# Performance work log

Hardware: AMD Instinct MI355X
Metric: run time of the kernel (lower is better)

## Reference

```python
import jax, jax.numpy as jnp
import numpy as np

GAMMA = 0.5  # RBF bandwidth, matches init_kwargs gamma


def setup_inputs() -> dict:
    key = jax.random.key(0)
    x = jax.random.normal(key, (8192, 64), dtype=jnp.float32)
    return {"x": x}


def reference(x):
    # Gram[i, j] = exp(-gamma * ||x_i - x_j||^2), computed fully batched.
    # ||xi - xj||^2 = ||xi||^2 + ||xj||^2 - 2 <xi, xj>
    sq = jnp.sum(x * x, axis=-1)                      # [n]
    d2 = sq[:, None] + sq[None, :] - 2.0 * (x @ x.T)  # [n, n]
    d2 = jnp.maximum(d2, 0.0)                         # numerical floor
    out = jnp.exp(-GAMMA * d2)                        # [n, n]
    n = x.shape[0]
    return out.reshape(n, -1)
```

## Files before the change

### kernel.cpp

```cpp
#include <hip/hip_runtime.h>


#define GAMMA 0.5f

typedef __attribute__((ext_vector_type(8))) _Float16 half8;
typedef __attribute__((ext_vector_type(4))) float f32x4;

__global__ __launch_bounds__(256) void quant_kernel(const float* __restrict__ x,
                                                    unsigned short* __restrict__ H,
                                                    float* __restrict__ sq) {
    int tid = blockIdx.x * 256 + threadIdx.x;
    int row = tid >> 4, c4 = tid & 15;
    float4 v = ((const float4*)x)[tid];
    float e[4] = {v.x, v.y, v.z, v.w};
    unsigned short hb[4];
    float s = 0.f;
    #pragma unroll
    for (int i = 0; i < 4; ++i) {
        _Float16 h = (_Float16)e[i];
        float hf = (float)h;
        s = fmaf(hf, hf, s);
        hb[i] = __builtin_bit_cast(unsigned short, h);
    }
    int rr = row & 127;
    size_t base = (size_t)(row >> 7) * 16384;
    int b = (rr * 128 + c4 * 8) ^ ((rr & 7) << 4);
    uint2 hw = {(unsigned)hb[0] | ((unsigned)hb[1] << 16),
                (unsigned)hb[2] | ((unsigned)hb[3] << 16)};
    *(uint2*)((char*)H + base + b) = hw;
    s += __shfl_xor(s, 1); s += __shfl_xor(s, 2);
    s += __shfl_xor(s, 4); s += __shfl_xor(s, 8);
    if (c4 == 0) sq[row] = s;
}

__global__ __launch_bounds__(256, 4) void rbf_mfma12(const unsigned short* __restrict__ H,
                                                     const float* __restrict__ sq,
                                                     float* __restrict__ out, int N) {
    __shared__ __align__(16) char smem[32768];
    unsigned short* Ah = (unsigned short*)smem;
    unsigned short* Bh = (unsigned short*)(smem + 16384);

    const int tid = threadIdx.x;
    const int i0 = blockIdx.y * 128, j0 = blockIdx.x * 128;
    const int w = tid >> 6, lane = tid & 63;
    const int fr = lane & 15, kg = lane >> 4;
    const int wr = w * 32;

    {
        const uint4* ga = (const uint4*)(H + (size_t)i0 * 64);
        const uint4* gb = (const uint4*)(H + (size_t)j0 * 64);
        #pragma unroll
        for (int t = 0; t < 4; ++t) {
            ((uint4*)Ah)[t * 256 + tid] = ga[t * 256 + tid];
            ((uint4*)Bh)[t * 256 + tid] = gb[t * 256 + tid];
        }
    }
    __syncthreads();

    f32x4 acc[2][8];
    #pragma unroll
    for (int p = 0; p < 2; ++p)
        #pragma unroll
        for (int q = 0; q < 8; ++q) acc[p][q] = (f32x4)(0.f);

    #pragma unroll
    for (int ks = 0; ks < 2; ++ks) {
        const int kb = ks * 64 + kg * 16;
        half8 ah[2], bh[8];
        #pragma unroll
        for (int p = 0; p < 2; ++p) {
            int R = wr + p * 16 + fr;
            int off = (R * 128 + kb) ^ ((R & 7) << 4);
            ah[p] = *(const half8*)((const char*)Ah + off);
        }
        #pragma unroll
        for (int q = 0; q < 8; ++q) {
            int R = q * 16 + fr;
            int off = (R * 128 + kb) ^ ((R & 7) << 4);
            bh[q] = *(const half8*)((const char*)Bh + off);
        }
        #pragma unroll
        for (int p = 0; p < 2; ++p)
            #pragma unroll
            for (int q = 0; q < 8; ++q)
                acc[p][q] = __builtin_amdgcn_mfma_f32_16x16x32_f16(bh[q], ah[p], acc[p][q], 0, 0, 0);
    }

    __syncthreads();
    float* wbuf = (float*)smem + w * 2048;

    #pragma unroll
    for (int p = 0; p < 2; ++p) {
        float sa = sq[i0 + wr + p * 16 + fr];
        #pragma unroll
        for (int q = 0; q < 8; ++q) {
            int c = q * 16 + kg * 4;
            float4 sb = *(const float4*)&sq[j0 + c];
            f32x4 a = acc[p][q];
            f32x4 r;
            r[0] = __expf(-GAMMA * fmaxf(fmaf(-2.f, a[0], sa + sb.x), 0.f));
            r[1] = __expf(-GAMMA * fmaxf(fmaf(-2.f, a[1], sa + sb.y), 0.f));
            r[2] = __expf(-GAMMA * fmaxf(fmaf(-2.f, a[2], sa + sb.z), 0.f));
            r[3] = __expf(-GAMMA * fmaxf(fmaf(-2.f, a[3], sa + sb.w), 0.f));
            *(f32x4*)&wbuf[fr * 128 + (c ^ ((fr & 7) << 2))] = r;
        }
        const int half = lane >> 5, lc = lane & 31;
        #pragma unroll
        for (int i = 0; i < 8; ++i) {
            int rl = i * 2 + half;
            f32x4 v = *(const f32x4*)&wbuf[rl * 128 + ((lc * 4) ^ ((rl & 7) << 2))];
            int grow = i0 + wr + p * 16 + rl;
            __builtin_nontemporal_store(v, (f32x4*)(out + (size_t)grow * N + j0 + lc * 4));
        }
    }
}

extern "C" void kernel_launch(void* const* d_in, const int* in_sizes, int n_in,
                              void* d_out, int out_size, void* d_ws, size_t ws_size,
                              hipStream_t stream) {
    (void)n_in; (void)ws_size; (void)out_size;
    const float* x = (const float*)d_in[0];
    float* out = (float*)d_out;
    const int K = 64;
    const int N = in_sizes[0] / K;

    unsigned short* H = (unsigned short*)d_ws;
    float* sq = (float*)(H + (size_t)N * K);

    quant_kernel<<<dim3(N * K / 4 / 256), dim3(256), 0, stream>>>(x, H, sq);
    rbf_mfma12<<<dim3(N / 128, N / 128), dim3(256), 0, stream>>>(H, sq, out, N);
}
```

Before: 55.91 us.

## Reshape tiles to 64x256 and write full 1KB output rows per wave

Changes the block tile from 128x128 to 64 rows by 256 columns. Each wave now computes a 16x256 strip, with a single A fragment reused across 16 MFMAs. The epilogue stages 8 rows at a time in LDS so each store instruction writes a contiguous 1KB row segment. Nontemporal stores become regular stores, and sched barriers plus an explicit lgkmcnt wait order the LDS phases. The B tile load doubles while the A tile halves, and the LDS footprint grows to 40KB, which may cut occupancy.

```diff
diff --git a/kernel.cpp b/kernel.cpp
--- a/kernel.cpp
+++ b/kernel.cpp
@@ -33,84 +33,78 @@
     if (c4 == 0) sq[row] = s;
 }
 
-__global__ __launch_bounds__(256, 4) void rbf_mfma12(const unsigned short* __restrict__ H,
+__global__ __launch_bounds__(256, 4) void rbf_mfma14(const unsigned short* __restrict__ H,
                                                      const float* __restrict__ sq,
                                                      float* __restrict__ out, int N) {
-    __shared__ __align__(16) char smem[32768];
+    __shared__ __align__(16) char smem[40960];
     unsigned short* Ah = (unsigned short*)smem;
-    unsigned short* Bh = (unsigned short*)(smem + 16384);
+    unsigned short* Bh = (unsigned short*)(smem + 8192);
 
     const int tid = threadIdx.x;
-    const int i0 = blockIdx.y * 128, j0 = blockIdx.x * 128;
+    const int i0 = blockIdx.y * 64, j0 = blockIdx.x * 256;
     const int w = tid >> 6, lane = tid & 63;
     const int fr = lane & 15, kg = lane >> 4;
-    const int wr = w * 32;
 
     {
         const uint4* ga = (const uint4*)(H + (size_t)i0 * 64);
         const uint4* gb = (const uint4*)(H + (size_t)j0 * 64);
         #pragma unroll
-        for (int t = 0; t < 4; ++t) {
+        for (int t = 0; t < 2; ++t)
             ((uint4*)Ah)[t * 256 + tid] = ga[t * 256 + tid];
+        #pragma unroll
+        for (int t = 0; t < 8; ++t)
             ((uint4*)Bh)[t * 256 + tid] = gb[t * 256 + tid];
-        }
     }
     __syncthreads();
 
-    f32x4 acc[2][8];
+    f32x4 acc[16];
     #pragma unroll
-    for (int p = 0; p < 2; ++p)
-        #pragma unroll
-        for (int q = 0; q < 8; ++q) acc[p][q] = (f32x4)(0.f);
+    for (int q = 0; q < 16; ++q) acc[q] = (f32x4)(0.f);
 
     #pragma unroll
     for (int ks = 0; ks < 2; ++ks) {
         const int kb = ks * 64 + kg * 16;
-        half8 ah[2], bh[8];
+        int Ra = w * 16 + fr;
+        half8 ah = *(const half8*)((const char*)Ah + ((Ra * 128 + kb) ^ ((Ra & 7) << 4)));
         #pragma unroll
-        for (int p = 0; p < 2; ++p) {
-            int R = wr + p * 16 + fr;
-            int off = (R * 128 + kb) ^ ((R & 7) << 4);
-            ah[p] = *(const half8*)((const char*)Ah + off);
+        for (int q = 0; q < 16; ++q) {
+            int R = q * 16 + fr;
+            int off = (((R & 127) * 128 + kb) ^ ((R & 7) << 4)) + ((R >> 7) << 14);
+            half8 bh = *(const half8*)((const char*)Bh + off);
+            acc[q] = __builtin_amdgcn_mfma_f32_16x16x32_f16(bh, ah, acc[q], 0, 0, 0);
         }
-        #pragma unroll
-        for (int q = 0; q < 8; ++q) {
-            int R = q * 16 + fr;
-            int off = (R * 128 + kb) ^ ((R & 7) << 4);
-            bh[q] = *(const half8*)((const char*)Bh + off);
-        }
-        #pragma unroll
-        for (int p = 0; p < 2; ++p)
-            #pragma unroll
-            for (int q = 0; q < 8; ++q)
-                acc[p][q] = __builtin_amdgcn_mfma_f32_16x16x32_f16(bh[q], ah[p], acc[p][q], 0, 0, 0);
     }
 
     __syncthreads();
     float* wbuf = (float*)smem + w * 2048;
 
+    const float sa = sq[i0 + w * 16 + fr];
     #pragma unroll
-    for (int p = 0; p < 2; ++p) {
-        float sa = sq[i0 + wr + p * 16 + fr];
+    for (int h = 0; h < 2; ++h) {
+        asm volatile("" ::: "memory");
+        __builtin_amdgcn_sched_barrier(0);
+        if ((fr >> 3) == h) {
+            int rl = fr & 7;
+            #pragma unroll
+            for (int q = 0; q < 16; ++q) {
+                int c = q * 16 + kg * 4;
+                float4 sb = *(const float4*)&sq[j0 + c];
+                f32x4 a = acc[q];
+                f32x4 r;
+                r[0] = __expf(-GAMMA * fmaxf(fmaf(-2.f, a[0], sa + sb.x), 0.f));
+                r[1] = __expf(-GAMMA * fmaxf(fmaf(-2.f, a[1], sa + sb.y), 0.f));
+                r[2] = __expf(-GAMMA * fmaxf(fmaf(-2.f, a[2], sa + sb.z), 0.f));
+                r[3] = __expf(-GAMMA * fmaxf(fmaf(-2.f, a[3], sa + sb.w), 0.f));
+                *(f32x4*)&wbuf[rl * 256 + (c ^ (rl << 2))] = r;
+            }
+        }
+        asm volatile("s_waitcnt lgkmcnt(0)" ::: "memory");
+        __builtin_amdgcn_sched_barrier(0);
         #pragma unroll
-        for (int q = 0; q < 8; ++q) {
-            int c = q * 16 + kg * 4;
-            float4 sb = *(const float4*)&sq[j0 + c];
-            f32x4 a = acc[p][q];
-            f32x4 r;
-            r[0] = __expf(-GAMMA * fmaxf(fmaf(-2.f, a[0], sa + sb.x), 0.f));
-            r[1] = __expf(-GAMMA * fmaxf(fmaf(-2.f, a[1], sa + sb.y), 0.f));
-            r[2] = __expf(-GAMMA * fmaxf(fmaf(-2.f, a[2], sa + sb.z), 0.f));
-            r[3] = __expf(-GAMMA * fmaxf(fmaf(-2.f, a[3], sa + sb.w), 0.f));
-            *(f32x4*)&wbuf[fr * 128 + (c ^ ((fr & 7) << 2))] = r;
-        }
-        const int half = lane >> 5, lc = lane & 31;
-        #pragma unroll
-        for (int i = 0; i < 8; ++i) {
-            int rl = i * 2 + half;
-            f32x4 v = *(const f32x4*)&wbuf[rl * 128 + ((lc * 4) ^ ((rl & 7) << 2))];
-            int grow = i0 + wr + p * 16 + rl;
-            __builtin_nontemporal_store(v, (f32x4*)(out + (size_t)grow * N + j0 + lc * 4));
+        for (int rl = 0; rl < 8; ++rl) {
+            f32x4 v = *(const f32x4*)&wbuf[rl * 256 + ((lane * 4) ^ (rl << 2))];
+            int grow = i0 + w * 16 + h * 8 + rl;
+            *(f32x4*)(out + (size_t)grow * N + j0 + lane * 4) = v;
         }
     }
 }
@@ -128,5 +122,5 @@
     float* sq = (float*)(H + (size_t)N * K);
 
     quant_kernel<<<dim3(N * K / 4 / 256), dim3(256), 0, stream>>>(x, H, sq);
-    rbf_mfma12<<<dim3(N / 128, N / 128), dim3(256), 0, stream>>>(H, sq, out, N);
+    rbf_mfma14<<<dim3(N / 256, N / 64), dim3(256), 0, stream>>>(H, sq, out, N);
 }
```

After: 66.01 us. 1.18x slower.
